# Performance work log

Hardware: AMD Instinct MI355X
Metric: run time of the kernel (lower is better)

Reference implementation:

```python
import jax, jax.numpy as jnp
import numpy as np

EMB_DIM = 256
NUM_EMB = 2048
COM_COEF = 0.25


def setup_inputs() -> dict:
    key = jax.random.key(0)
    k1, k2 = jax.random.split(key)
    x = jax.random.normal(k1, (64, 32, 32, EMB_DIM), dtype=jnp.float32)
    # VarianceScaling(uniform) over (emb_dim, num_emb): limit = sqrt(3*scale/fan_in)
    limit = float(np.sqrt(3.0 / EMB_DIM))
    codebook = jax.random.uniform(k2, (EMB_DIM, NUM_EMB), dtype=jnp.float32,
                                  minval=-limit, maxval=limit)
    return {"x": x, "codebook": codebook}


def reference(x, codebook):
    original_shape = x.shape
    flat = jnp.reshape(x, (-1, EMB_DIM))  # [N, D]
    sim = jnp.matmul(flat, codebook)
    dists = (jnp.sum(jnp.square(flat), axis=-1, keepdims=True)
             + jnp.sum(jnp.square(codebook), axis=0)
             - 2.0 * sim)
    indexes = jnp.argmin(dists, axis=-1)  # [N]
    encodings = jax.nn.one_hot(indexes, NUM_EMB, dtype=flat.dtype)  # [N, num_emb]
    quantized = jnp.matmul(encodings, codebook.T)  # [N, D]
    quantized = jnp.reshape(quantized, original_shape)

    latent_loss = jnp.square(jax.lax.stop_gradient(x) - quantized)
    commitment_loss = jnp.square(jax.lax.stop_gradient(quantized) - x)
    loss = jnp.mean(latent_loss + COM_COEF * commitment_loss)

    # straight-through estimator
    quantized_st = x + jax.lax.stop_gradient(quantized - x)

    avg_probs = jnp.mean(encodings, axis=0)
    perplexity = jnp.exp(-jnp.sum(avg_probs * jnp.log(avg_probs + 1e-10)))
    return quantized_st, loss, perplexity
```

## Files before the change

### kernel.cpp

```cpp
#include <hip/hip_runtime.h>
#include <hip/hip_fp16.h>
#include <math.h>

#define EMB_DIM 256
#define NUM_EMB 2048
#define N_ROWS  65536
#define N_ELEM  16777216
#define EPS_GAP 8e-3f

#define IDX_OFF    0
#define XSQ_OFF    65536
#define ESQ_OFF    131072
#define ESQH_OFF   133120
#define HIST_OFF   135168
#define BKT_OFF    137216
#define CNT_OFF    137472
#define FLG_OFF    137473
#define CBT_OFF    262144
#define CBTH_OFF   786432

typedef __attribute__((ext_vector_type(8))) _Float16 half8;
typedef __attribute__((ext_vector_type(4))) float f32x4;
typedef unsigned int u32;

__device__ __forceinline__ void gl_lds16(const void* g, void* l) {
    __builtin_amdgcn_global_load_lds(
        (const __attribute__((address_space(1))) u32*)g,
        (__attribute__((address_space(3))) u32*)l, 16, 0, 0);
}

__global__ __launch_bounds__(256) void esq_k(const float* __restrict__ cb,
                                             float* __restrict__ esq,
                                             float* __restrict__ esqh) {
    int e = blockIdx.x * 256 + threadIdx.x;
    float s0 = 0.f, s1 = 0.f, s2 = 0.f, s3 = 0.f;
    float h0 = 0.f, h1 = 0.f, h2 = 0.f, h3 = 0.f;
    for (int d = 0; d < EMB_DIM; d += 4) {
        float c0 = cb[(d + 0) * NUM_EMB + e];
        float c1 = cb[(d + 1) * NUM_EMB + e];
        float c2 = cb[(d + 2) * NUM_EMB + e];
        float c3 = cb[(d + 3) * NUM_EMB + e];
        s0 = fmaf(c0, c0, s0); s1 = fmaf(c1, c1, s1);
        s2 = fmaf(c2, c2, s2); s3 = fmaf(c3, c3, s3);
        float q0 = __half2float(__float2half(c0));
        float q1 = __half2float(__float2half(c1));
        float q2 = __half2float(__float2half(c2));
        float q3 = __half2float(__float2half(c3));
        h0 = fmaf(q0, q0, h0); h1 = fmaf(q1, q1, h1);
        h2 = fmaf(q2, q2, h2); h3 = fmaf(q3, q3, h3);
    }
    esq[e]  = (s0 + s1) + (s2 + s3);
    esqh[e] = (h0 + h1) + (h2 + h3);
}

__global__ __launch_bounds__(256) void prep_cbt(const float* __restrict__ cb,
                                                float* __restrict__ cbT,
                                                __half* __restrict__ cbTh) {
    __shared__ float lt[64][65];
    int t = threadIdx.x;
    int et = (blockIdx.x & 31) * 64;
    int dt = (blockIdx.x >> 5) * 64;
    #pragma unroll
    for (int p = 0; p < 4; ++p) {
        int d  = p * 16 + (t >> 4);
        int e4 = (t & 15) * 4;
        const float4 v = *(const float4*)&cb[(dt + d) * NUM_EMB + et + e4];
        lt[d][e4] = v.x; lt[d][e4 + 1] = v.y; lt[d][e4 + 2] = v.z; lt[d][e4 + 3] = v.w;
    }
    __syncthreads();
    #pragma unroll
    for (int p = 0; p < 4; ++p) {
        int e  = p * 16 + (t >> 4);
        int d4 = (t & 15) * 4;
        float a[4] = {lt[d4][e], lt[d4 + 1][e], lt[d4 + 2][e], lt[d4 + 3][e]};
        *(float4*)&cbT[(et + e) * EMB_DIM + dt + d4] = make_float4(a[0], a[1], a[2], a[3]);
        unsigned short hb[4];
        #pragma unroll
        for (int i = 0; i < 4; ++i)
            hb[i] = __half_as_ushort(__float2half(a[i]));
        *(ushort4*)&cbTh[(et + e) * EMB_DIM + dt + d4] = make_ushort4(hb[0], hb[1], hb[2], hb[3]);
    }
}

__global__ __launch_bounds__(256) void prep_x(const float* __restrict__ x,
                                              __half* __restrict__ xh,
                                              float* __restrict__ xsq) {
    int t = threadIdx.x;
    int row = blockIdx.x * 4 + (t >> 6);
    int c = (t & 63) * 4;
    const float4 v = *(const float4*)&x[row * EMB_DIM + c];
    float a[4] = {v.x, v.y, v.z, v.w};
    unsigned short hb[4];
    float s = 0.f;
    #pragma unroll
    for (int i = 0; i < 4; ++i) {
        hb[i] = __half_as_ushort(__float2half(a[i]));
        s = fmaf(a[i], a[i], s);
    }
    *(ushort4*)&xh[row * EMB_DIM + c] = make_ushort4(hb[0], hb[1], hb[2], hb[3]);
    #pragma unroll
    for (int o = 32; o > 0; o >>= 1) s += __shfl_down(s, o, 64);
    if ((t & 63) == 0) xsq[row] = s;
}

#define BUFH 10240
__global__ __launch_bounds__(256, 2) void argmin_mfma(
    const __half* __restrict__ xh_, const __half* __restrict__ cbh_,
    const float* __restrict__ esqh,
    int* __restrict__ idx_out, int* __restrict__ cnt, int* __restrict__ flg) {

    __shared__ _Float16 ldsbuf[3 * BUFH];
    _Float16* lds = ldsbuf;

    const _Float16* xh  = (const _Float16*)xh_;
    const _Float16* cbh = (const _Float16*)cbh_;

    const int t = threadIdx.x;
    const int w = t >> 6, L = t & 63;
    const int wn = w * 64;
    const int lm = L & 15, lq = L >> 4;
    const int ph = (lm >> 1) & 3;
    const int rowbase = blockIdx.x * 64;

    const int srow = L >> 2;
    const int sq   = (L & 3) ^ ((L >> 3) & 3);

    const _Float16* pa  = xh + (size_t)(rowbase + w * 16 + srow) * EMB_DIM + sq * 8;
    const _Float16* pb0 = cbh + (size_t)(w * 16 + srow) * EMB_DIM + sq * 8;
    const int oA = (w * 16) * 32;
    const int oB = 2048 + (w * 16) * 32;

    float best[16], b2[16];
    int   bi[16];
    #pragma unroll
    for (int s = 0; s < 16; ++s) { best[s] = 3.4e38f; b2[s] = 3.4e38f; bi[s] = 0; }

    #define STAGE(gs, bb) do {                                                   \
        const int nnt_ = (gs) >> 3, nkt_ = (gs) & 7;                             \
        const int ko_  = nkt_ * 32;                                              \
        const _Float16* pb_ = pb0 + ((size_t)nnt_ * 256) * EMB_DIM + ko_;        \
        gl_lds16(pa + ko_, (bb) + oA);                                           \
        gl_lds16(pb_ +   0 * EMB_DIM, (bb) + oB +    0);                         \
        gl_lds16(pb_ +  64 * EMB_DIM, (bb) + oB + 2048);                         \
        gl_lds16(pb_ + 128 * EMB_DIM, (bb) + oB + 4096);                         \
        gl_lds16(pb_ + 192 * EMB_DIM, (bb) + oB + 6144);                         \
    } while (0)

    STAGE(0, lds);
    STAGE(1, lds + BUFH);

    for (int nt = 0; nt < 8; ++nt) {
        float eq[4];
        #pragma unroll
        for (int g = 0; g < 4; ++g)
            eq[g] = esqh[nt * 256 + wn + g * 16 + lm];

        f32x4 acc[4][4];
        #pragma unroll
        for (int f = 0; f < 4; ++f)
            #pragma unroll
            for (int g = 0; g < 4; ++g)
                acc[f][g] = (f32x4){0.f, 0.f, 0.f, 0.f};

        for (int kt = 0; kt < 8; ++kt) {
            const int step = nt * 8 + kt;

            __builtin_amdgcn_sched_barrier(0);
            if (step < 63) {
                asm volatile("s_waitcnt vmcnt(5)" ::: "memory");
            } else {
                asm volatile("s_waitcnt vmcnt(0)" ::: "memory");
            }
            __builtin_amdgcn_s_barrier();
            __builtin_amdgcn_sched_barrier(0);

            if (step < 62)
                STAGE(step + 2, lds + ((step + 2) % 3) * BUFH);

            const _Float16* sa = lds + (step % 3) * BUFH;
            const _Float16* sb = sa + 2048;

            half8 ah[4], bh[4];
            #pragma unroll
            for (int f = 0; f < 4; ++f)
                ah[f] = *(const half8*)&sa[(f * 16 + lm) * 32 + ((lq ^ ph) * 8)];
            #pragma unroll
            for (int g = 0; g < 4; ++g)
                bh[g] = *(const half8*)&sb[(wn + g * 16 + lm) * 32 + ((lq ^ ph) * 8)];

            __builtin_amdgcn_s_setprio(1);
            #pragma unroll
            for (int f = 0; f < 4; ++f)
                #pragma unroll
                for (int g = 0; g < 4; ++g)
                    acc[f][g] = __builtin_amdgcn_mfma_f32_16x16x32_f16(ah[f], bh[g], acc[f][g], 0, 0, 0);
            __builtin_amdgcn_s_setprio(0);
        }

        #pragma unroll
        for (int g = 0; g < 4; ++g) {
            int col = nt * 256 + wn + g * 16 + lm;
            #pragma unroll
            for (int f = 0; f < 4; ++f)
                #pragma unroll
                for (int r = 0; r < 4; ++r) {
                    int s = f * 4 + r;
                    float v = fmaf(-2.0f, acc[f][g][r], eq[g]);
                    float bo = best[s];
                    b2[s]   = fminf(b2[s], fmaxf(bo, v));
                    best[s] = fminf(bo, v);
                    bi[s]   = (v < bo) ? col : bi[s];
                }
        }
    }
    #undef STAGE

    __syncthreads();
    float* smemf = (float*)ldsbuf;
    float* rd = smemf;
    int*   ri = (int*)(smemf + 4160);
    float* r2 = smemf + 8320;
    #pragma unroll
    for (int f = 0; f < 4; ++f)
        #pragma unroll
        for (int r = 0; r < 4; ++r) {
            int row = f * 16 + lq * 4 + r;
            int c = w * 16 + lm;
            rd[row * 65 + c] = best[f * 4 + r];
            ri[row * 65 + c] = bi[f * 4 + r];
            r2[row * 65 + c] = b2[f * 4 + r];
        }
    __syncthreads();
    if (t < 64) {
        int row = t;
        float g1 = rd[row * 65]; int gi = ri[row * 65]; float g2 = r2[row * 65];
        for (int c = 1; c < 64; ++c) {
            float d = rd[row * 65 + c]; int ic = ri[row * 65 + c]; float d2 = r2[row * 65 + c];
            if (d < g1 || (d == g1 && ic < gi)) { g2 = fminf(g1, d2); g1 = d; gi = ic; }
            else g2 = fminf(g2, d);
        }
        idx_out[rowbase + row] = gi;
        if (g2 - g1 < EPS_GAP) {
            int p = atomicAdd(cnt, 1);
            flg[p] = rowbase + row;
        }
    }
}

__global__ __launch_bounds__(256) void fallback_k(const float* __restrict__ x,
                                                  const float* __restrict__ cb,
                                                  const float* __restrict__ xsq,
                                                  const float* __restrict__ esq,
                                                  const int* __restrict__ cnt,
                                                  const int* __restrict__ rows,
                                                  int* __restrict__ idx) {
    __shared__ float xr[4][256];
    __shared__ float sd[4][256];
    __shared__ int   si[4][256];
    int t = threadIdx.x;
    int n = *cnt;
    for (int base = blockIdx.x * 4; base < n; base += gridDim.x * 4) {
        int rws[4];
        #pragma unroll
        for (int r = 0; r < 4; ++r) {
            int fi = base + r;
            rws[r] = rows[(fi < n) ? fi : (n - 1)];
        }
        __syncthreads();
        #pragma unroll
        for (int r = 0; r < 4; ++r) xr[r][t] = x[(size_t)rws[r] * EMB_DIM + t];
        __syncthreads();

        float bd[4]; int bidx[4];
        #pragma unroll
        for (int r = 0; r < 4; ++r) { bd[r] = 3.4e38f; bidx[r] = 0x7fffffff; }

        for (int j = 0; j < 8; ++j) {
            int e = j * 256 + t;
            float s0[4], s1[4], s2[4], s3[4];
            #pragma unroll
            for (int r = 0; r < 4; ++r) { s0[r] = 0.f; s1[r] = 0.f; s2[r] = 0.f; s3[r] = 0.f; }
            for (int d = 0; d < EMB_DIM; d += 4) {
                float c0 = cb[(size_t)(d + 0) * NUM_EMB + e];
                float c1 = cb[(size_t)(d + 1) * NUM_EMB + e];
                float c2 = cb[(size_t)(d + 2) * NUM_EMB + e];
                float c3 = cb[(size_t)(d + 3) * NUM_EMB + e];
                #pragma unroll
                for (int r = 0; r < 4; ++r) {
                    const float4 xv = *(const float4*)&xr[r][d];
                    s0[r] = fmaf(xv.x, c0, s0[r]);
                    s1[r] = fmaf(xv.y, c1, s1[r]);
                    s2[r] = fmaf(xv.z, c2, s2[r]);
                    s3[r] = fmaf(xv.w, c3, s3[r]);
                }
            }
            float eqv = esq[e];
            #pragma unroll
            for (int r = 0; r < 4; ++r) {
                float sim = (s0[r] + s1[r]) + (s2[r] + s3[r]);
                float dd = (xsq[rws[r]] + eqv) - 2.0f * sim;
                if (dd < bd[r]) { bd[r] = dd; bidx[r] = e; }
            }
        }
        #pragma unroll
        for (int r = 0; r < 4; ++r) { sd[r][t] = bd[r]; si[r][t] = bidx[r]; }
        __syncthreads();
        for (int r = 0; r < 4; ++r) {
            for (int stp = 128; stp > 0; stp >>= 1) {
                if (t < stp) {
                    if (sd[r][t + stp] < sd[r][t] ||
                        (sd[r][t + stp] == sd[r][t] && si[r][t + stp] < si[r][t])) {
                        sd[r][t] = sd[r][t + stp]; si[r][t] = si[r][t + stp];
                    }
                }
                __syncthreads();
            }
        }
        if (t == 0) {
            #pragma unroll
            for (int r = 0; r < 4; ++r) idx[rws[r]] = si[r][0];
        }
    }
}

__global__ __launch_bounds__(256) void quant_k(const float* __restrict__ x,
                                               const float* __restrict__ cbT,
                                               const int* __restrict__ idx,
                                               float* __restrict__ out,
                                               float* __restrict__ bkt,
                                               int* __restrict__ hist) {
    int t = threadIdx.x;
    int row = blockIdx.x * 4 + (t >> 6);
    int c = (t & 63) * 4;
    int e = idx[row];
    const float4 q  = *(const float4*)&cbT[(size_t)e * EMB_DIM + c];
    const float4 xv = *(const float4*)&x[(size_t)row * EMB_DIM + c];
    float4 o;
    o.x = xv.x + (q.x - xv.x); o.y = xv.y + (q.y - xv.y);
    o.z = xv.z + (q.z - xv.z); o.w = xv.w + (q.w - xv.w);
    *(float4*)&out[(size_t)row * EMB_DIM + c] = o;
    float dx = xv.x - q.x, dy = xv.y - q.y, dz = xv.z - q.z, dw = xv.w - q.w;
    float val = fmaf(dx, dx, 0.f);
    val = fmaf(dy, dy, val);
    val = fmaf(dz, dz, val);
    val = fmaf(dw, dw, val);
    #pragma unroll
    for (int o2 = 32; o2 > 0; o2 >>= 1) val += __shfl_down(val, o2, 64);
    if ((t & 63) == 0) {
        atomicAdd(&bkt[row & 255], val);
        atomicAdd(&hist[e], 1);
    }
}

__global__ __launch_bounds__(256) void final_k(const float* __restrict__ bkt,
                                               const int* __restrict__ hist,
                                               float* __restrict__ out) {
    int t = threadIdx.x;
    double ls = (double)bkt[t];
    double ps = 0.0;
    for (int i = t; i < NUM_EMB; i += 256) {
        double p = (double)hist[i] / (double)N_ROWS;
        ps += p * log(p + 1e-10);
    }
    __shared__ double sdd[256], spp[256];
    sdd[t] = ls; spp[t] = ps;
    __syncthreads();
    for (int s = 128; s > 0; s >>= 1) {
        if (t < s) { sdd[t] += sdd[t + s]; spp[t] += spp[t + s]; }
        __syncthreads();
    }
    if (t == 0) {
        out[N_ELEM + 0] = (float)(1.25 * sdd[0] / (double)N_ELEM);
        out[N_ELEM + 1] = (float)exp(-spp[0]);
    }
}

extern "C" void kernel_launch(void* const* d_in, const int* in_sizes, int n_in,
                              void* d_out, int out_size, void* d_ws, size_t ws_size,
                              hipStream_t stream) {
    const float* x  = (const float*)d_in[0];
    const float* cb = (const float*)d_in[1];
    float* out = (float*)d_out;

    float* ws_f = (float*)d_ws;
    int*   ws_i = (int*)d_ws;
    int*   idx  = ws_i + IDX_OFF;
    float* xsq  = ws_f + XSQ_OFF;
    float* esq  = ws_f + ESQ_OFF;
    float* esqh = ws_f + ESQH_OFF;
    int*   hist = ws_i + HIST_OFF;
    float* bkt  = ws_f + BKT_OFF;
    int*   cnt  = ws_i + CNT_OFF;
    int*   flg  = ws_i + FLG_OFF;
    float* cbT  = ws_f + CBT_OFF;
    __half* cbTh = (__half*)(ws_f + CBTH_OFF);

    __half* xh = (__half*)d_out;

    hipMemsetAsync((char*)d_ws + (size_t)HIST_OFF * 4, 0,
                   (NUM_EMB + 256 + 1) * sizeof(float), stream);

    esq_k<<<NUM_EMB / 256, 256, 0, stream>>>(cb, esq, esqh);
    prep_cbt<<<128, 256, 0, stream>>>(cb, cbT, cbTh);
    prep_x<<<N_ROWS / 4, 256, 0, stream>>>(x, xh, xsq);
    argmin_mfma<<<N_ROWS / 64, 256, 0, stream>>>(xh, cbTh, esqh, idx, cnt, flg);
    fallback_k<<<512, 256, 0, stream>>>(x, cb, xsq, esq, cnt, flg, idx);
    quant_k<<<N_ROWS / 4, 256, 0, stream>>>(x, cbT, idx, out, bkt, hist);
    final_k<<<1, 256, 0, stream>>>(bkt, hist, out);
}
```

Baseline: 450.3 us.

## Merge prep kernels and switch argmin to double-buffered K64 stages

```diff
diff --git a/kernel.cpp b/kernel.cpp
--- a/kernel.cpp
+++ b/kernel.cpp
@@ -29,87 +29,85 @@
         (__attribute__((address_space(3))) u32*)l, 16, 0, 0);
 }
 
-__global__ __launch_bounds__(256) void esq_k(const float* __restrict__ cb,
-                                             float* __restrict__ esq,
-                                             float* __restrict__ esqh) {
-    int e = blockIdx.x * 256 + threadIdx.x;
-    float s0 = 0.f, s1 = 0.f, s2 = 0.f, s3 = 0.f;
-    float h0 = 0.f, h1 = 0.f, h2 = 0.f, h3 = 0.f;
-    for (int d = 0; d < EMB_DIM; d += 4) {
-        float c0 = cb[(d + 0) * NUM_EMB + e];
-        float c1 = cb[(d + 1) * NUM_EMB + e];
-        float c2 = cb[(d + 2) * NUM_EMB + e];
-        float c3 = cb[(d + 3) * NUM_EMB + e];
-        s0 = fmaf(c0, c0, s0); s1 = fmaf(c1, c1, s1);
-        s2 = fmaf(c2, c2, s2); s3 = fmaf(c3, c3, s3);
-        float q0 = __half2float(__float2half(c0));
-        float q1 = __half2float(__float2half(c1));
-        float q2 = __half2float(__float2half(c2));
-        float q3 = __half2float(__float2half(c3));
-        h0 = fmaf(q0, q0, h0); h1 = fmaf(q1, q1, h1);
-        h2 = fmaf(q2, q2, h2); h3 = fmaf(q3, q3, h3);
-    }
-    esq[e]  = (s0 + s1) + (s2 + s3);
-    esqh[e] = (h0 + h1) + (h2 + h3);
-}
-
-__global__ __launch_bounds__(256) void prep_cbt(const float* __restrict__ cb,
-                                                float* __restrict__ cbT,
-                                                __half* __restrict__ cbTh) {
+__global__ __launch_bounds__(256) void prep_all(
+    const float* __restrict__ x, const float* __restrict__ cb,
+    float* __restrict__ esq, float* __restrict__ esqh,
+    float* __restrict__ cbT, __half* __restrict__ cbTh,
+    __half* __restrict__ xh, float* __restrict__ xsq) {
     __shared__ float lt[64][65];
-    int t = threadIdx.x;
-    int et = (blockIdx.x & 31) * 64;
-    int dt = (blockIdx.x >> 5) * 64;
-    #pragma unroll
-    for (int p = 0; p < 4; ++p) {
-        int d  = p * 16 + (t >> 4);
-        int e4 = (t & 15) * 4;
-        const float4 v = *(const float4*)&cb[(dt + d) * NUM_EMB + et + e4];
-        lt[d][e4] = v.x; lt[d][e4 + 1] = v.y; lt[d][e4 + 2] = v.z; lt[d][e4 + 3] = v.w;
-    }
-    __syncthreads();
-    #pragma unroll
-    for (int p = 0; p < 4; ++p) {
-        int e  = p * 16 + (t >> 4);
-        int d4 = (t & 15) * 4;
-        float a[4] = {lt[d4][e], lt[d4 + 1][e], lt[d4 + 2][e], lt[d4 + 3][e]};
-        *(float4*)&cbT[(et + e) * EMB_DIM + dt + d4] = make_float4(a[0], a[1], a[2], a[3]);
+    const int bid = blockIdx.x;
+    const int t = threadIdx.x;
+    if (bid < 8) {
+        int e = bid * 256 + t;
+        float s0 = 0.f, s1 = 0.f, s2 = 0.f, s3 = 0.f;
+        float h0 = 0.f, h1 = 0.f, h2 = 0.f, h3 = 0.f;
+        for (int d = 0; d < EMB_DIM; d += 4) {
+            float c0 = cb[(d + 0) * NUM_EMB + e];
+            float c1 = cb[(d + 1) * NUM_EMB + e];
+            float c2 = cb[(d + 2) * NUM_EMB + e];
+            float c3 = cb[(d + 3) * NUM_EMB + e];
+            s0 = fmaf(c0, c0, s0); s1 = fmaf(c1, c1, s1);
+            s2 = fmaf(c2, c2, s2); s3 = fmaf(c3, c3, s3);
+            float q0 = __half2float(__float2half(c0));
+            float q1 = __half2float(__float2half(c1));
+            float q2 = __half2float(__float2half(c2));
+            float q3 = __half2float(__float2half(c3));
+            h0 = fmaf(q0, q0, h0); h1 = fmaf(q1, q1, h1);
+            h2 = fmaf(q2, q2, h2); h3 = fmaf(q3, q3, h3);
+        }
+        esq[e]  = (s0 + s1) + (s2 + s3);
+        esqh[e] = (h0 + h1) + (h2 + h3);
+    } else if (bid < 136) {
+        int b = bid - 8;
+        int et = (b & 31) * 64;
+        int dt = (b >> 5) * 64;
+        #pragma unroll
+        for (int p = 0; p < 4; ++p) {
+            int d  = p * 16 + (t >> 4);
+            int e4 = (t & 15) * 4;
+            const float4 v = *(const float4*)&cb[(dt + d) * NUM_EMB + et + e4];
+            lt[d][e4] = v.x; lt[d][e4 + 1] = v.y; lt[d][e4 + 2] = v.z; lt[d][e4 + 3] = v.w;
+        }
+        __syncthreads();
+        #pragma unroll
+        for (int p = 0; p < 4; ++p) {
+            int e  = p * 16 + (t >> 4);
+            int d4 = (t & 15) * 4;
+            float a[4] = {lt[d4][e], lt[d4 + 1][e], lt[d4 + 2][e], lt[d4 + 3][e]};
+            *(float4*)&cbT[(et + e) * EMB_DIM + dt + d4] = make_float4(a[0], a[1], a[2], a[3]);
+            unsigned short hb[4];
+            #pragma unroll
+            for (int i = 0; i < 4; ++i)
+                hb[i] = __half_as_ushort(__float2half(a[i]));
+            *(ushort4*)&cbTh[(et + e) * EMB_DIM + dt + d4] = make_ushort4(hb[0], hb[1], hb[2], hb[3]);
+        }
+    } else {
+        int b = bid - 136;
+        int row = b * 4 + (t >> 6);
+        int c = (t & 63) * 4;
+        const float4 v = *(const float4*)&x[row * EMB_DIM + c];
+        float a[4] = {v.x, v.y, v.z, v.w};
         unsigned short hb[4];
-        #pragma unroll
-        for (int i = 0; i < 4; ++i)
+        float s = 0.f;
+        #pragma unroll
+        for (int i = 0; i < 4; ++i) {
             hb[i] = __half_as_ushort(__float2half(a[i]));
-        *(ushort4*)&cbTh[(et + e) * EMB_DIM + dt + d4] = make_ushort4(hb[0], hb[1], hb[2], hb[3]);
-    }
-}
-
-__global__ __launch_bounds__(256) void prep_x(const float* __restrict__ x,
-                                              __half* __restrict__ xh,
-                                              float* __restrict__ xsq) {
-    int t = threadIdx.x;
-    int row = blockIdx.x * 4 + (t >> 6);
-    int c = (t & 63) * 4;
-    const float4 v = *(const float4*)&x[row * EMB_DIM + c];
-    float a[4] = {v.x, v.y, v.z, v.w};
-    unsigned short hb[4];
-    float s = 0.f;
-    #pragma unroll
-    for (int i = 0; i < 4; ++i) {
-        hb[i] = __half_as_ushort(__float2half(a[i]));
-        s = fmaf(a[i], a[i], s);
-    }
-    *(ushort4*)&xh[row * EMB_DIM + c] = make_ushort4(hb[0], hb[1], hb[2], hb[3]);
-    #pragma unroll
-    for (int o = 32; o > 0; o >>= 1) s += __shfl_down(s, o, 64);
-    if ((t & 63) == 0) xsq[row] = s;
-}
-
-#define BUFH 10240
+            s = fmaf(a[i], a[i], s);
+        }
+        *(ushort4*)&xh[row * EMB_DIM + c] = make_ushort4(hb[0], hb[1], hb[2], hb[3]);
+        #pragma unroll
+        for (int o = 32; o > 0; o >>= 1) s += __shfl_down(s, o, 64);
+        if ((t & 63) == 0) xsq[row] = s;
+    }
+}
+
+#define BUFH 20480
 __global__ __launch_bounds__(256, 2) void argmin_mfma(
     const __half* __restrict__ xh_, const __half* __restrict__ cbh_,
     const float* __restrict__ esqh,
     int* __restrict__ idx_out, int* __restrict__ cnt, int* __restrict__ flg) {
 
-    __shared__ _Float16 ldsbuf[3 * BUFH];
+    __shared__ _Float16 ldsbuf[2 * BUFH];
     _Float16* lds = ldsbuf;
 
     const _Float16* xh  = (const _Float16*)xh_;
@@ -128,26 +126,30 @@
     const _Float16* pa  = xh + (size_t)(rowbase + w * 16 + srow) * EMB_DIM + sq * 8;
     const _Float16* pb0 = cbh + (size_t)(w * 16 + srow) * EMB_DIM + sq * 8;
     const int oA = (w * 16) * 32;
-    const int oB = 2048 + (w * 16) * 32;
+    const int oB = (w * 16) * 32;
 
     float best[16], b2[16];
     int   bi[16];
     #pragma unroll
     for (int s = 0; s < 16; ++s) { best[s] = 3.4e38f; b2[s] = 3.4e38f; bi[s] = 0; }
 
-    #define STAGE(gs, bb) do {                                                   \
-        const int nnt_ = (gs) >> 3, nkt_ = (gs) & 7;                             \
-        const int ko_  = nkt_ * 32;                                              \
-        const _Float16* pb_ = pb0 + ((size_t)nnt_ * 256) * EMB_DIM + ko_;        \
-        gl_lds16(pa + ko_, (bb) + oA);                                           \
-        gl_lds16(pb_ +   0 * EMB_DIM, (bb) + oB +    0);                         \
-        gl_lds16(pb_ +  64 * EMB_DIM, (bb) + oB + 2048);                         \
-        gl_lds16(pb_ + 128 * EMB_DIM, (bb) + oB + 4096);                         \
-        gl_lds16(pb_ + 192 * EMB_DIM, (bb) + oB + 6144);                         \
+    #define STAGE(S_, bb) do {                                                   \
+        const int nnt_ = (S_) >> 2;                                              \
+        const int km_  = ((S_) & 3) * 64;                                        \
+        const _Float16* pb_ = pb0 + (size_t)nnt_ * 256 * EMB_DIM + km_;          \
+        gl_lds16(pa + km_,                 (bb) + oA);                           \
+        gl_lds16(pa + km_ + 32,            (bb) + 2048 + oA);                    \
+        gl_lds16(pb_ +   0 * EMB_DIM,      (bb) + 4096 + oB);                    \
+        gl_lds16(pb_ +  64 * EMB_DIM,      (bb) + 4096 + oB + 2048);             \
+        gl_lds16(pb_ + 128 * EMB_DIM,      (bb) + 4096 + oB + 4096);             \
+        gl_lds16(pb_ + 192 * EMB_DIM,      (bb) + 4096 + oB + 6144);             \
+        gl_lds16(pb_ +   0 * EMB_DIM + 32, (bb) + 12288 + oB);                   \
+        gl_lds16(pb_ +  64 * EMB_DIM + 32, (bb) + 12288 + oB + 2048);            \
+        gl_lds16(pb_ + 128 * EMB_DIM + 32, (bb) + 12288 + oB + 4096);            \
+        gl_lds16(pb_ + 192 * EMB_DIM + 32, (bb) + 12288 + oB + 6144);            \
     } while (0)
 
     STAGE(0, lds);
-    STAGE(1, lds + BUFH);
 
     for (int nt = 0; nt < 8; ++nt) {
         float eq[4];
@@ -162,38 +164,44 @@
             for (int g = 0; g < 4; ++g)
                 acc[f][g] = (f32x4){0.f, 0.f, 0.f, 0.f};
 
-        for (int kt = 0; kt < 8; ++kt) {
-            const int step = nt * 8 + kt;
+        for (int mt = 0; mt < 4; ++mt) {
+            const int S = nt * 4 + mt;
 
             __builtin_amdgcn_sched_barrier(0);
-            if (step < 63) {
-                asm volatile("s_waitcnt vmcnt(5)" ::: "memory");
-            } else {
-                asm volatile("s_waitcnt vmcnt(0)" ::: "memory");
-            }
+            asm volatile("s_waitcnt vmcnt(0)" ::: "memory");
             __builtin_amdgcn_s_barrier();
             __builtin_amdgcn_sched_barrier(0);
 
-            if (step < 62)
-                STAGE(step + 2, lds + ((step + 2) % 3) * BUFH);
-
-            const _Float16* sa = lds + (step % 3) * BUFH;
-            const _Float16* sb = sa + 2048;
-
-            half8 ah[4], bh[4];
-            #pragma unroll
-            for (int f = 0; f < 4; ++f)
-                ah[f] = *(const half8*)&sa[(f * 16 + lm) * 32 + ((lq ^ ph) * 8)];
-            #pragma unroll
-            for (int g = 0; g < 4; ++g)
-                bh[g] = *(const half8*)&sb[(wn + g * 16 + lm) * 32 + ((lq ^ ph) * 8)];
-
-            __builtin_amdgcn_s_setprio(1);
-            #pragma unroll
-            for (int f = 0; f < 4; ++f)
+            if (S < 31)
+                STAGE(S + 1, lds + ((S + 1) & 1) * BUFH);
+
+            const _Float16* bb = lds + (S & 1) * BUFH;
+
+            half8 ah[2][4], bh[2][4];
+            #pragma unroll
+            for (int h = 0; h < 2; ++h)
+                #pragma unroll
+                for (int f = 0; f < 4; ++f)
+                    ah[h][f] = *(const half8*)&bb[h * 2048 + (f * 16 + lm) * 32 + ((lq ^ ph) * 8)];
+            #pragma unroll
+            for (int h = 0; h < 2; ++h)
                 #pragma unroll
                 for (int g = 0; g < 4; ++g)
-                    acc[f][g] = __builtin_amdgcn_mfma_f32_16x16x32_f16(ah[f], bh[g], acc[f][g], 0, 0, 0);
+                    bh[h][g] = *(const half8*)&bb[4096 + h * 8192 + (wn + g * 16 + lm) * 32 + ((lq ^ ph) * 8)];
+
+            asm volatile("s_waitcnt lgkmcnt(0)" ::: "memory");
+            __builtin_amdgcn_sched_barrier(0);
+            __builtin_amdgcn_s_barrier();
+            __builtin_amdgcn_sched_barrier(0);
+
+            __builtin_amdgcn_s_setprio(1);
+            #pragma unroll
+            for (int h = 0; h < 2; ++h)
+                #pragma unroll
+                for (int f = 0; f < 4; ++f)
+                    #pragma unroll
+                    for (int g = 0; g < 4; ++g)
+                        acc[f][g] = __builtin_amdgcn_mfma_f32_16x16x32_f16(ah[h][f], bh[h][g], acc[f][g], 0, 0, 0);
             __builtin_amdgcn_s_setprio(0);
         }
 
@@ -400,9 +408,7 @@
     hipMemsetAsync((char*)d_ws + (size_t)HIST_OFF * 4, 0,
                    (NUM_EMB + 256 + 1) * sizeof(float), stream);
 
-    esq_k<<<NUM_EMB / 256, 256, 0, stream>>>(cb, esq, esqh);
-    prep_cbt<<<128, 256, 0, stream>>>(cb, cbT, cbTh);
-    prep_x<<<N_ROWS / 4, 256, 0, stream>>>(x, xh, xsq);
+    prep_all<<<8 + 128 + N_ROWS / 4, 256, 0, stream>>>(x, cb, esq, esqh, cbT, cbTh, xh, xsq);
     argmin_mfma<<<N_ROWS / 64, 256, 0, stream>>>(xh, cbTh, esqh, idx, cnt, flg);
     fallback_k<<<512, 256, 0, stream>>>(x, cb, xsq, esq, cnt, flg, idx);
     quant_k<<<N_ROWS / 4, 256, 0, stream>>>(x, cbT, idx, out, bkt, hist);
```

After: 431.6 us. -4.1%, faster.
